# Performance work log

Measured on AMD Instinct MI355X. Metric: run time of the kernel, lower is better.

## Reference

```python
import jax, jax.numpy as jnp
import numpy as np

B, N, NI, H, QK, A = 1, 256, 64, 256, 128, 11
M = B * N

def _lstm_cell(x, h, c, w_ih, w_hh, b_ih, b_hh):
    # PyTorch LSTMCell gate order: i, f, g, o
    g = x @ w_ih.T + b_ih + h @ w_hh.T + b_hh
    i, f, gg, o = jnp.split(g, 4, axis=-1)
    c2 = jax.nn.sigmoid(f) * c + jax.nn.sigmoid(i) * jnp.tanh(gg)
    return jax.nn.sigmoid(o) * jnp.tanh(c2), c2

def _run_lstm(xs, w_ih, w_hh, b_ih, b_hh, reverse):
    # xs: (T, Bm, I); one direction of nn.LSTM with zero initial state
    Bm, Hh = xs.shape[1], w_hh.shape[1]
    def step(carry, x):
        h2, c2 = _lstm_cell(x, carry[0], carry[1], w_ih, w_hh, b_ih, b_hh)
        return (h2, c2), h2
    init = (jnp.zeros((Bm, Hh), xs.dtype), jnp.zeros((Bm, Hh), xs.dtype))
    return jax.lax.scan(step, init, xs, reverse=reverse)[1]

def setup_inputs():
    key = jax.random.key(0)
    ks = jax.random.split(key, 28)
    s = 0.1
    p = lambda k, sh: jax.random.normal(k, sh, jnp.float32) * s
    u = jax.random.uniform(ks[1], (M - 1, M, 2), jnp.float32, 1e-6, 1.0)
    return {
        "x": jax.random.normal(ks[0], (B, N, NI), jnp.float32),
        "h_in": jnp.zeros((M, H), jnp.float32),
        "c_in": jnp.zeros((M, H), jnp.float32),
        "gumbel": -jnp.log(-jnp.log(u)),
        "enc_w": p(ks[2], (H, NI)), "enc_b": p(ks[3], (H,)),
        "cell_w_ih": p(ks[4], (4 * H, H)), "cell_w_hh": p(ks[5], (4 * H, H)),
        "cell_b_ih": p(ks[6], (4 * H,)), "cell_b_hh": p(ks[7], (4 * H,)),
        "lf_w_ih": p(ks[8], (8 * H, 2 * H)), "lf_w_hh": p(ks[9], (8 * H, 2 * H)),
        "lf_b_ih": p(ks[10], (8 * H,)), "lf_b_hh": p(ks[11], (8 * H,)),
        "lr_w_ih": p(ks[12], (8 * H, 2 * H)), "lr_w_hh": p(ks[13], (8 * H, 2 * H)),
        "lr_b_ih": p(ks[14], (8 * H,)), "lr_b_hh": p(ks[15], (8 * H,)),
        "lin_w": p(ks[16], (2, 4 * H)), "lin_b": p(ks[17], (2,)),
        "wq_w": p(ks[18], (QK, H)), "wq_b": p(ks[19], (QK,)),
        "wk_w": p(ks[20], (QK, H)), "wk_b": p(ks[21], (QK,)),
        "val_w": p(ks[22], (1, 2 * H)), "val_b": p(ks[23], (1,)),
        "head_w": p(ks[24], (A, 2 * H)), "head_b": p(ks[25], (A,)),
    }

def _forward(x, h_in, c_in, gumbel, enc_w, enc_b, cell_w_ih, cell_w_hh, cell_b_ih, cell_b_hh,
             lf_w_ih, lf_w_hh, lf_b_ih, lf_b_hh, lr_w_ih, lr_w_hh, lr_b_ih, lr_b_hh,
             lin_w, lin_b, wq_w, wq_b, wk_w, wk_b, val_w, val_b, head_w, head_b):
    enc = x @ enc_w.T + enc_b                    # (B, N, H)
    inp = enc.reshape(M, H)
    h, c = _lstm_cell(inp, h_in, c_in, cell_w_ih, cell_w_hh, cell_b_ih, cell_b_hh)
    # idx[a, t] = t-th other agent for agent a (skips self) -- replaces the nested Python loops
    ar = jnp.arange(M - 1)[None, :]
    idx = ar + (ar >= jnp.arange(M)[:, None])    # (M, M-1) int
    pair = jnp.concatenate([jnp.broadcast_to(h[:, None, :], (M, M - 1, H)), h[idx]], axis=-1)
    hai = pair.transpose(1, 0, 2)                # (M-1, M, 2H), seq-major like torch stack(dim=1)
    y = jnp.concatenate([
        _run_lstm(hai, lf_w_ih, lf_w_hh, lf_b_ih, lf_b_hh, False),
        _run_lstm(hai, lr_w_ih, lr_w_hh, lr_b_ih, lr_b_hh, True)], axis=-1)  # (M-1, M, 4H)
    logits = y @ lin_w.T + lin_b                 # (M-1, M, 2)
    # hard gumbel-softmax (tau=1) with straight-through estimator
    ysoft = jax.nn.softmax(logits + gumbel, axis=-1)
    oh = jax.nn.one_hot(jnp.argmax(ysoft, axis=-1), 2, dtype=ysoft.dtype)
    gs = oh + ysoft - jax.lax.stop_gradient(ysoft)
    hard = gs[..., 1].transpose(1, 0)            # (M, M-1): narrow(dim=2,1,1) + permute + squeeze
    nz = jnp.count_nonzero(hard).astype(jnp.float32)
    d1 = nz / (N * N)
    d2 = nz / (N * (N - 1))
    q = h @ wq_w.T + wq_b
    k = h @ wk_w.T + wk_b
    sa = (q @ k.T) * (1.0 / float(np.sqrt(QK)))  # (M, M)
    sa = jnp.take_along_axis(sa, idx, axis=1) * hard   # drop diagonal, gate
    attn = jax.nn.softmax(sa, axis=1) * hard
    # agent_mask is all ones here (no 'alive_mask' in info), so masking is identity
    comm = jnp.einsum('mt,mth->mh', attn, h[idx])      # (M, H)
    val = jnp.concatenate([h, comm], axis=-1) @ val_w.T + val_b  # (M, 1)
    h3 = h.reshape(B, N, H)
    c3 = comm.reshape(B, N, H)
    act = jax.nn.log_softmax(jnp.concatenate([h3, c3], axis=-1) @ head_w.T + head_b, axis=-1)
    return act, val, h, c, jnp.stack([d1, d2])

def reference(x, h_in, c_in, gumbel, enc_w, enc_b, cell_w_ih, cell_w_hh, cell_b_ih, cell_b_hh,
              lf_w_ih, lf_w_hh, lf_b_ih, lf_b_hh, lr_w_ih, lr_w_hh, lr_b_ih, lr_b_hh,
              lin_w, lin_b, wq_w, wq_b, wk_w, wk_b, val_w, val_b, head_w, head_b):
    return _forward(x, h_in, c_in, gumbel, enc_w, enc_b, cell_w_ih, cell_w_hh, cell_b_ih, cell_b_hh,
                    lf_w_ih, lf_w_hh, lf_b_ih, lf_b_hh, lr_w_ih, lr_w_hh, lr_b_ih, lr_b_hh,
                    lin_w, lin_b, wq_w, wq_b, wk_w, wk_b, val_w, val_b, head_w, head_b)
```

## Files before the change

### kernel.cpp

```cpp
#include <hip/hip_runtime.h>
#include <hip/hip_bf16.h>

typedef float f32x4  __attribute__((ext_vector_type(4)));
typedef short s16x4  __attribute__((ext_vector_type(4)));
typedef short s16x8  __attribute__((ext_vector_type(8)));
typedef __bf16 bf16x8 __attribute__((ext_vector_type(8)));
typedef unsigned int u32;
typedef unsigned long long u64;

#define DEVI static __device__ __forceinline__

DEVI short f2bf(float f){
  u32 u = __builtin_bit_cast(u32,f);
  u += 0x7fffu + ((u>>16)&1u);
  return (short)(u>>16);
}
DEVI float sigm(float x){ return 1.f/(1.f+__expf(-x)); }
DEVI float tanh_(float x){ return 1.f - 2.f/(1.f+__expf(2.f*x)); }

DEVI bf16x8 ldbf8(const short* p){ return __builtin_bit_cast(bf16x8, *(const s16x8*)p); }

DEVI f32x4 cld16(const void* p){
  f32x4 r;
  asm volatile("global_load_dwordx4 %0, %1, off sc0 sc1" : "=v"(r) : "v"(p) : "memory");
  return r;
}
DEVI void cst8(void* p, u64 v){
  asm volatile("global_store_dwordx2 %0, %1, off sc0 sc1" :: "v"(p), "v"(v) : "memory");
}
DEVI void cst4(int* p, int v){
  asm volatile("global_store_dword %0, %1, off sc0 sc1" :: "v"(p), "v"(v) : "memory");
}
DEVI int cld4(const int* p){
  int r;
  asm volatile("global_load_dword %0, %1, off sc0 sc1\n\ts_waitcnt vmcnt(0)"
               : "=v"(r) : "v"(p) : "memory");
  return r;
}

#define NSTEP 255

#define WS_H1F      0u
#define WS_H1BF     262144u
#define WS_ABUF     393216u
#define WS_CELLW    655360u
#define WS_WIH      1703936u
#define WS_WPACK    5898240u
#define WS_GATES1   10092544u
#define WS_GX       11141120u
#define WS_HBUF     19529728u
#define WS_LDIFF    20578304u
#define WS_Q        28934144u
#define WS_K        29065216u
#define WS_SA       29196288u
#define WS_HARD     29458432u
#define WS_FLAGS    29719552u
#define WS_NZ       29723648u

__global__ void k_pack(const float* __restrict__ lf_whh, const float* __restrict__ lr_whh,
                       const float* __restrict__ cwih, const float* __restrict__ cwhh,
                       const float* __restrict__ lf_wih, const float* __restrict__ lr_wih,
                       short* __restrict__ wpack, short* __restrict__ cellw, short* __restrict__ wih)
{
  int bx = blockIdx.x, tid = threadIdx.x;
  if (bx < 1024) {
    int idx = bx*256 + tid;
    int lane = idx & 63;
    int kk   = (idx>>6)&15;
    int ct   = (idx>>10)&3;
    int w    = (idx>>12)&3;
    int hb8  = (idx>>14)&7;
    int d    = (idx>>17)&1;
    const float* W = d ? lr_whh : lf_whh;
    int wrow = 512*w + hb8*64 + ct*16 + (lane&15);
    short v[8];
    #pragma unroll
    for (int jj=0;jj<8;++jj){
      int k = 32*kk + 8*(lane>>4) + jj;
      v[jj] = f2bf(W[(size_t)wrow*512 + k]);
    }
    s16x8 o;
    #pragma unroll
    for (int jj=0;jj<8;++jj) o[jj] = v[jj];
    *(s16x8*)(wpack + (size_t)idx*8) = o;
  } else if (bx < 3072) {
    int e = (bx-1024)*256 + tid;
    int cg = e>>9, k = e&511;
    float val = (k<256) ? cwih[cg*256 + k] : cwhh[cg*256 + (k-256)];
    cellw[e] = f2bf(val);
  } else {
    int e = (bx-3072)*256 + tid;
    int d = e>>20, r = e & 1048575;
    const float* W = d ? lr_wih : lf_wih;
    wih[e] = f2bf(W[r]);
  }
}

__global__ void k1a(const float* __restrict__ x, const float* __restrict__ enc_w,
                    const float* __restrict__ enc_b, const float* __restrict__ h_in,
                    short* __restrict__ abuf)
{
  __shared__ float xs[64];
  int b = blockIdx.x, u = threadIdx.x;
  if (u < 64) xs[u] = x[b*64 + u];
  __syncthreads();
  float acc = enc_b[u];
  #pragma unroll 8
  for (int j=0;j<64;++j) acc += xs[j]*enc_w[u*64+j];
  abuf[b*512 + u]       = f2bf(acc);
  abuf[b*512 + 256 + u] = f2bf(h_in[b*256 + u]);
}

__global__ void k1b(const short* __restrict__ abuf, const short* __restrict__ cellw,
                    float* __restrict__ gates1)
{
  int tid = threadIdx.x, w = tid>>6, l = tid&63;
  int m0 = (blockIdx.x&3)*64 + 32*(w&1);
  int n0 = (blockIdx.x>>2)*64 + 32*(w>>1);
  int arow = l&15, ag = l>>4;
  f32x4 acc[2][2] = {};
  #pragma unroll 4
  for (int kk=0; kk<16; ++kk){
    int ko = 32*kk + 8*ag;
    bf16x8 a0 = ldbf8(abuf + (size_t)(m0 + arow)*512 + ko);
    bf16x8 a1 = ldbf8(abuf + (size_t)(m0 + 16 + arow)*512 + ko);
    bf16x8 b0 = ldbf8(cellw + (size_t)(n0 + arow)*512 + ko);
    bf16x8 b1 = ldbf8(cellw + (size_t)(n0 + 16 + arow)*512 + ko);
    acc[0][0] = __builtin_amdgcn_mfma_f32_16x16x32_bf16(a0,b0,acc[0][0],0,0,0);
    acc[0][1] = __builtin_amdgcn_mfma_f32_16x16x32_bf16(a0,b1,acc[0][1],0,0,0);
    acc[1][0] = __builtin_amdgcn_mfma_f32_16x16x32_bf16(a1,b0,acc[1][0],0,0,0);
    acc[1][1] = __builtin_amdgcn_mfma_f32_16x16x32_bf16(a1,b1,acc[1][1],0,0,0);
  }
  #pragma unroll
  for (int rt=0;rt<2;++rt)
    #pragma unroll
    for (int ct=0;ct<2;++ct)
      #pragma unroll
      for (int reg=0;reg<4;++reg)
        gates1[(size_t)(m0 + 16*rt + 4*ag + reg)*1024 + n0 + 16*ct + arow] = acc[rt][ct][reg];
}

__global__ void k1c(const float* __restrict__ gates1, const float* __restrict__ bih,
                    const float* __restrict__ bhh, const float* __restrict__ c_in,
                    float* __restrict__ out_h, float* __restrict__ out_c,
                    float* __restrict__ h1f, short* __restrict__ h1bf)
{
  int b = blockIdx.x, u = threadIdx.x;
  const float* g = gates1 + (size_t)b*1024;
  float iv = g[u]     + bih[u]     + bhh[u];
  float fv = g[256+u] + bih[256+u] + bhh[256+u];
  float gv = g[512+u] + bih[512+u] + bhh[512+u];
  float ov = g[768+u] + bih[768+u] + bhh[768+u];
  float c = sigm(fv)*c_in[b*256+u] + sigm(iv)*tanh_(gv);
  float h = sigm(ov)*tanh_(c);
  out_h[b*256+u] = h; out_c[b*256+u] = c;
  h1f[b*256+u] = h;   h1bf[b*256+u] = f2bf(h);
}

__global__ void k_qk(const float* __restrict__ h1, const float* __restrict__ wq_w,
                     const float* __restrict__ wq_b, const float* __restrict__ wk_w,
                     const float* __restrict__ wk_b, float* __restrict__ q, float* __restrict__ k)
{
  __shared__ float hrow[256];
  int b = blockIdx.x, u = threadIdx.x;
  hrow[u] = h1[b*256+u];
  hrow[u+128] = h1[b*256+u+128];
  __syncthreads();
  const float* W  = blockIdx.y ? wk_w : wq_w;
  const float* bb = blockIdx.y ? wk_b : wq_b;
  float* out = blockIdx.y ? k : q;
  float acc = bb[u];
  #pragma unroll 8
  for (int j=0;j<256;++j) acc += hrow[j]*W[u*256+j];
  out[b*128+u] = acc;
}

__global__ void k_sa(const float* __restrict__ q, const float* __restrict__ k, float* __restrict__ sa)
{
  __shared__ float qrow[128];
  int b = blockIdx.x, j = threadIdx.x;
  if (j < 128) qrow[j] = q[b*128+j];
  __syncthreads();
  float acc = 0.f;
  #pragma unroll 8
  for (int kk=0;kk<128;++kk) acc += qrow[kk]*k[j*128+kk];
  sa[b*256+j] = acc * 0.08838834764831845f;
}

__global__ void k_gx(const short* __restrict__ h1bf, const short* __restrict__ wih,
                     const float* __restrict__ lf_bih, const float* __restrict__ lf_bhh,
                     const float* __restrict__ lr_bih, const float* __restrict__ lr_bhh,
                     float* __restrict__ gx)
{
  int z = blockIdx.y, d = z>>1, half = z&1;
  int tid = threadIdx.x, w = tid>>6, l = tid&63;
  int m0 = (blockIdx.x&3)*64 + 32*(w&1);
  int n0 = (blockIdx.x>>2)*64 + 32*(w>>1);
  int arow = l&15, ag = l>>4;
  const short* Bb = wih + (size_t)d*2048*512 + 256*half;
  f32x4 acc[2][2] = {};
  #pragma unroll 4
  for (int kk=0;kk<8;++kk){
    int ko = 32*kk + 8*ag;
    bf16x8 a0 = ldbf8(h1bf + (size_t)(m0 + arow)*256 + ko);
    bf16x8 a1 = ldbf8(h1bf + (size_t)(m0 + 16 + arow)*256 + ko);
    bf16x8 b0 = ldbf8(Bb + (size_t)(n0 + arow)*512 + ko);
    bf16x8 b1 = ldbf8(Bb + (size_t)(n0 + 16 + arow)*512 + ko);
    acc[0][0] = __builtin_amdgcn_mfma_f32_16x16x32_bf16(a0,b0,acc[0][0],0,0,0);
    acc[0][1] = __builtin_amdgcn_mfma_f32_16x16x32_bf16(a0,b1,acc[0][1],0,0,0);
    acc[1][0] = __builtin_amdgcn_mfma_f32_16x16x32_bf16(a1,b0,acc[1][0],0,0,0);
    acc[1][1] = __builtin_amdgcn_mfma_f32_16x16x32_bf16(a1,b1,acc[1][1],0,0,0);
  }
  const float* bi = d ? lr_bih : lf_bih;
  const float* bh = d ? lr_bhh : lf_bhh;
  float* out = gx + (size_t)z*256*2048;
  #pragma unroll
  for (int rt=0;rt<2;++rt)
    #pragma unroll
    for (int ct=0;ct<2;++ct){
      int cg = n0 + 16*ct + arow;
      float bias = (half==0) ? (bi[cg] + bh[cg]) : 0.f;
      #pragma unroll
      for (int reg=0;reg<4;++reg)
        out[(size_t)(m0 + 16*rt + 4*ag + reg)*2048 + cg] = acc[rt][ct][reg] + bias;
    }
}

__global__ __launch_bounds__(256,1) void k_rec(
  const short* __restrict__ wpack, const float* __restrict__ gx,
  short* __restrict__ hbuf, float* __restrict__ ldiff,
  const float* __restrict__ lin_w, int* __restrict__ flags)
{
  __shared__ short h_lds[2][16*512];
  __shared__ float glds[2][4][16][68];
  const int tid = threadIdx.x;
  const int w = tid>>6, l = tid&63;
  const int bid = blockIdx.x;
  const int d   = bid>>7;
  const int g16 = (bid>>3)&15;
  const int hb8 = bid&7;
  const int r0  = g16*16;
  const int grp = d*16 + g16;

  bf16x8 breg[4][16];
  {
    const short* wp = wpack + (size_t)(((d*8+hb8)*4 + w)*4)*16*64*8 + (size_t)l*8;
    #pragma unroll
    for (int ct=0;ct<4;++ct)
      #pragma unroll
      for (int kk=0;kk<16;++kk)
        breg[ct][kk] = ldbf8(wp + (size_t)(ct*16+kk)*64*8);
  }

  const int r_e = tid>>4;
  const int j4  = (tid&15)*4;
  const int rg_e = r0 + r_e;
  float gx1c[16], ldwc[4];
  {
    const float* g1 = gx + ((size_t)(d*2)*256 + rg_e)*2048 + hb8*64 + j4;
    #pragma unroll
    for (int g=0;g<4;++g){
      f32x4 v = *(const f32x4*)(g1 + g*512);
      gx1c[g*4+0]=v.x; gx1c[g*4+1]=v.y; gx1c[g*4+2]=v.z; gx1c[g*4+3]=v.w;
    }
    #pragma unroll
    for (int jj=0;jj<4;++jj){
      int col = d*512 + hb8*64 + j4 + jj;
      ldwc[jj] = lin_w[1024+col] - lin_w[col];
    }
  }
  float c_st[4] = {0.f,0.f,0.f,0.f};
  int* slots  = flags + grp*32;
  int* myslot = slots + hb8*4 + w;
  const float* gx2base = gx + (size_t)(d*2+1)*256*2048 + hb8*64 + j4;

  const int s_row = tid>>4;
  const int c0    = tid&15;
  const int arow = l&15, ag = l>>4;

  for (int tau=0; tau<NSTEP; ++tau){
    const int t = d ? (254-tau) : tau;
    f32x4 x2r[4];
    {
      const float* g2 = gx2base + (size_t)(t + (t>=rg_e ? 1:0))*2048;
      #pragma unroll
      for (int g=0;g<4;++g) x2r[g] = *(const f32x4*)(g2 + g*512);
    }
    if (tau){
      int v = tau;
      do {
        if (l < 32) v = cld4(slots + l);
      } while (__any(v < tau));
    }
    const int p = tau&1;
    {
      const short* hsrc = hbuf + (size_t)((p*2+d)*256 + r0 + s_row)*512;
      f32x4 q[4];
      #pragma unroll
      for (int i=0;i<4;++i)
        q[i] = cld16(hsrc + (size_t)(c0 + 16*i)*8);
      asm volatile("s_waitcnt vmcnt(0)" ::: "memory");
      #pragma unroll
      for (int i=0;i<4;++i){
        int c = c0 + 16*i;
        int wb = (16*c) ^ ((s_row&15)<<4);
        *(f32x4*)((char*)h_lds[p] + s_row*1024 + wb) = q[i];
      }
    }
    __syncthreads();
    f32x4 acc[4] = {};
    #pragma unroll
    for (int kk=0;kk<16;++kk){
      int swz0 = (64*kk + 16*ag) ^ (arow<<4);
      bf16x8 a = __builtin_bit_cast(bf16x8, *(const s16x8*)((char*)h_lds[p] + arow*1024 + swz0));
      acc[0] = __builtin_amdgcn_mfma_f32_16x16x32_bf16(a,breg[0][kk],acc[0],0,0,0);
      acc[1] = __builtin_amdgcn_mfma_f32_16x16x32_bf16(a,breg[1][kk],acc[1],0,0,0);
      acc[2] = __builtin_amdgcn_mfma_f32_16x16x32_bf16(a,breg[2][kk],acc[2],0,0,0);
      acc[3] = __builtin_amdgcn_mfma_f32_16x16x32_bf16(a,breg[3][kk],acc[3],0,0,0);
    }
    #pragma unroll
    for (int ct=0;ct<4;++ct)
      #pragma unroll
      for (int reg=0;reg<4;++reg)
        glds[p][w][4*ag + reg][16*ct + arow] = acc[ct][reg];
    __syncthreads();
    {
      float gvals[16], hv[4];
      #pragma unroll
      for (int g=0; g<4; ++g){
        f32x4 mm = *(const f32x4*)&glds[p][g][r_e][j4];
        gvals[g*4+0] = mm.x + gx1c[g*4+0] + x2r[g].x;
        gvals[g*4+1] = mm.y + gx1c[g*4+1] + x2r[g].y;
        gvals[g*4+2] = mm.z + gx1c[g*4+2] + x2r[g].z;
        gvals[g*4+3] = mm.w + gx1c[g*4+3] + x2r[g].w;
      }
      #pragma unroll
      for (int jj=0;jj<4;++jj){
        float iv = sigm(gvals[jj]);
        float fv = sigm(gvals[4+jj]);
        float gg = tanh_(gvals[8+jj]);
        float ov = sigm(gvals[12+jj]);
        float cc = fv*c_st[jj] + iv*gg;
        c_st[jj] = cc;
        hv[jj] = ov*tanh_(cc);
      }
      short* hdst = hbuf + (size_t)(((p^1)*2+d)*256 + rg_e)*512 + hb8*64 + j4;
      u32 lo = (u32)(unsigned short)f2bf(hv[0]) | ((u32)(unsigned short)f2bf(hv[1])<<16);
      u32 hi = (u32)(unsigned short)f2bf(hv[2]) | ((u32)(unsigned short)f2bf(hv[3])<<16);
      cst8(hdst, (u64)lo | ((u64)hi << 32));
      asm volatile("s_waitcnt vmcnt(0)" ::: "memory");
      if (l==0)
        cst4(myslot, tau+1);
      float s = hv[0]*ldwc[0] + hv[1]*ldwc[1] + hv[2]*ldwc[2] + hv[3]*ldwc[3];
      s += __shfl_xor(s,1); s += __shfl_xor(s,2); s += __shfl_xor(s,4); s += __shfl_xor(s,8);
      if ((l&15)==0)
        ldiff[((size_t)t*16 + d*8 + hb8)*256 + rg_e] = s;
    }
  }
}

__global__ void k_hard(const float* __restrict__ ldiff, const float* __restrict__ lin_b,
                       const float* __restrict__ gumbel, float* __restrict__ hard,
                       int* __restrict__ nz)
{
  int t = blockIdx.x, b = threadIdx.x;
  float s = lin_b[1] - lin_b[0];
  #pragma unroll 8
  for (int k=0;k<16;++k) s += ldiff[((size_t)t*16 + k)*256 + b];
  const float* gp = gumbel + ((size_t)t*256 + b)*2;
  s += gp[1] - gp[0];
  int bit = (s > 0.f) ? 1 : 0;
  hard[(size_t)b*255 + t] = (float)bit;
  unsigned long long ball = __ballot(bit);
  __shared__ int cnt[4];
  if ((threadIdx.x & 63)==0) cnt[threadIdx.x>>6] = __popcll(ball);
  __syncthreads();
  if (threadIdx.x==0) atomicAdd(nz, cnt[0]+cnt[1]+cnt[2]+cnt[3]);
}

__global__ void k_attn(const float* __restrict__ h1, const float* __restrict__ sa,
                       const float* __restrict__ hard,
                       const float* __restrict__ val_w, const float* __restrict__ val_b,
                       const float* __restrict__ head_w, const float* __restrict__ head_b,
                       const int* __restrict__ nz,
                       float* __restrict__ out_act, float* __restrict__ out_val,
                       float* __restrict__ out_d)
{
  __shared__ float red[256];
  __shared__ float at[256];
  __shared__ float wred[4];
  __shared__ float logit[11];
  int b = blockIdx.x, u = threadIdx.x;
  float hd = 0.f, sc = -3.0e38f;
  if (u < 255){
    hd = hard[(size_t)b*255 + u];
    int jsel = u + (u>=b ? 1:0);
    sc = sa[b*256 + jsel] * hd;
  }
  red[u] = sc; __syncthreads();
  for (int st=128; st; st>>=1){ if (u<st) red[u] = fmaxf(red[u], red[u+st]); __syncthreads(); }
  float mx = red[0]; __syncthreads();
  float e = (u<255) ? __expf(sc - mx) : 0.f;
  red[u] = e; __syncthreads();
  for (int st=128; st; st>>=1){ if (u<st) red[u] += red[u+st]; __syncthreads(); }
  float inv = 1.f/red[0]; __syncthreads();
  at[u] = (u<255) ? e*inv*hd : 0.f;
  __syncthreads();
  float comm = 0.f;
  for (int t2=0; t2<255; ++t2){
    int jsel = t2 + (t2>=b ? 1:0);
    comm += at[t2] * h1[(size_t)jsel*256 + u];
  }
  float hb_ = h1[(size_t)b*256 + u];
  float pv = hb_*val_w[u] + comm*val_w[256+u];
  red[u] = pv; __syncthreads();
  for (int st=128; st; st>>=1){ if (u<st) red[u] += red[u+st]; __syncthreads(); }
  if (u==0) out_val[b] = red[0] + val_b[0];
  for (int a=0; a<11; ++a){
    float s = hb_*head_w[a*512+u] + comm*head_w[a*512+256+u];
    s += __shfl_xor(s,32); s += __shfl_xor(s,16); s += __shfl_xor(s,8);
    s += __shfl_xor(s,4);  s += __shfl_xor(s,2);  s += __shfl_xor(s,1);
    if ((u&63)==0) wred[u>>6] = s;
    __syncthreads();
    if (u==0) logit[a] = wred[0]+wred[1]+wred[2]+wred[3] + head_b[a];
    __syncthreads();
  }
  if (u==0){
    float m = logit[0];
    #pragma unroll
    for (int a=1;a<11;++a) m = fmaxf(m, logit[a]);
    float se = 0.f;
    #pragma unroll
    for (int a=0;a<11;++a) se += __expf(logit[a]-m);
    float ls = __logf(se);
    #pragma unroll
    for (int a=0;a<11;++a) out_act[(size_t)b*11 + a] = logit[a] - m - ls;
  }
  if (b==0 && u==0){
    float n = (float)(*nz);
    out_d[0] = n / 65536.f;
    out_d[1] = n / 65280.f;
  }
}

extern "C" void kernel_launch(void* const* d_in, const int* in_sizes, int n_in,
                              void* d_out, int out_size, void* d_ws, size_t ws_size,
                              hipStream_t stream)
{
  const float* x      = (const float*)d_in[0];
  const float* h_in   = (const float*)d_in[1];
  const float* c_in   = (const float*)d_in[2];
  const float* gumbel = (const float*)d_in[3];
  const float* enc_w  = (const float*)d_in[4];
  const float* enc_b  = (const float*)d_in[5];
  const float* cwih   = (const float*)d_in[6];
  const float* cwhh   = (const float*)d_in[7];
  const float* cbih   = (const float*)d_in[8];
  const float* cbhh   = (const float*)d_in[9];
  const float* lf_wih = (const float*)d_in[10];
  const float* lf_whh = (const float*)d_in[11];
  const float* lf_bih = (const float*)d_in[12];
  const float* lf_bhh = (const float*)d_in[13];
  const float* lr_wih = (const float*)d_in[14];
  const float* lr_whh = (const float*)d_in[15];
  const float* lr_bih = (const float*)d_in[16];
  const float* lr_bhh = (const float*)d_in[17];
  const float* lin_w  = (const float*)d_in[18];
  const float* lin_b  = (const float*)d_in[19];
  const float* wq_w   = (const float*)d_in[20];
  const float* wq_b   = (const float*)d_in[21];
  const float* wk_w   = (const float*)d_in[22];
  const float* wk_b   = (const float*)d_in[23];
  const float* val_w  = (const float*)d_in[24];
  const float* val_b  = (const float*)d_in[25];
  const float* head_w = (const float*)d_in[26];
  const float* head_b = (const float*)d_in[27];

  char* ws = (char*)d_ws;
  float* h1f   = (float*)(ws + WS_H1F);
  short* h1bf  = (short*)(ws + WS_H1BF);
  short* abuf  = (short*)(ws + WS_ABUF);
  short* cellw = (short*)(ws + WS_CELLW);
  short* wih   = (short*)(ws + WS_WIH);
  short* wpack = (short*)(ws + WS_WPACK);
  float* gates1= (float*)(ws + WS_GATES1);
  float* gx    = (float*)(ws + WS_GX);
  short* hbuf  = (short*)(ws + WS_HBUF);
  float* ldiff = (float*)(ws + WS_LDIFF);
  float* qb    = (float*)(ws + WS_Q);
  float* kb    = (float*)(ws + WS_K);
  float* sab   = (float*)(ws + WS_SA);
  float* hardb = (float*)(ws + WS_HARD);
  int*   flags = (int*)(ws + WS_FLAGS);
  int*   nz    = (int*)(ws + WS_NZ);

  float* out_act = (float*)d_out;
  float* out_val = out_act + 2816;
  float* out_h   = out_val + 256;
  float* out_c   = out_h + 65536;
  float* out_d   = out_c + 65536;

  hipMemsetAsync(flags, 0, 4100, stream);
  hipMemsetAsync(hbuf, 0, 1048576, stream);

  k_pack<<<11264, 256, 0, stream>>>(lf_whh, lr_whh, cwih, cwhh, lf_wih, lr_wih, wpack, cellw, wih);
  k1a <<<256, 256, 0, stream>>>(x, enc_w, enc_b, h_in, abuf);
  k1b <<<64, 256, 0, stream>>>(abuf, cellw, gates1);
  k1c <<<256, 256, 0, stream>>>(gates1, cbih, cbhh, c_in, out_h, out_c, h1f, h1bf);
  k_qk<<<dim3(256,2), 128, 0, stream>>>(h1f, wq_w, wq_b, wk_w, wk_b, qb, kb);
  k_sa<<<256, 256, 0, stream>>>(qb, kb, sab);
  k_gx<<<dim3(128,4), 256, 0, stream>>>(h1bf, wih, lf_bih, lf_bhh, lr_bih, lr_bhh, gx);
  k_rec<<<256, 256, 0, stream>>>(wpack, gx, hbuf, ldiff, lin_w, flags);
  k_hard<<<255, 256, 0, stream>>>(ldiff, lin_b, gumbel, hardb, nz);
  k_attn<<<256, 256, 0, stream>>>(h1f, sab, hardb, val_w, val_b, head_w, head_b, nz,
                                  out_act, out_val, out_d);
}
```

Before: 1.050 ms.

## Replace flag polling with checksum-tagged hidden-state validation in recurrent kernel

Drops the separate step counter flags in the recurrence and their ordering. Producers no longer wait for the hidden-state store to complete before raising a flag. Instead, each wave publishes an XOR checksum of its hidden-state block, salted with a per-step golden-ratio value. Consumers load the hidden-state data and tags together and spin until the recomputed checksums match. This removes one full store-wait-then-poll round trip per timestep. In exchange, correctness becomes probabilistic: a checksum collision could accept stale data, and a bounded spin limit silently proceeds with whatever was loaded.

```diff
diff --git a/kernel.cpp b/kernel.cpp
--- a/kernel.cpp
+++ b/kernel.cpp
@@ -25,19 +25,16 @@
   asm volatile("global_load_dwordx4 %0, %1, off sc0 sc1" : "=v"(r) : "v"(p) : "memory");
   return r;
 }
+DEVI u64 cld8(const void* p){
+  u64 r;
+  asm volatile("global_load_dwordx2 %0, %1, off sc0 sc1" : "=v"(r) : "v"(p) : "memory");
+  return r;
+}
 DEVI void cst8(void* p, u64 v){
   asm volatile("global_store_dwordx2 %0, %1, off sc0 sc1" :: "v"(p), "v"(v) : "memory");
 }
-DEVI void cst4(int* p, int v){
-  asm volatile("global_store_dword %0, %1, off sc0 sc1" :: "v"(p), "v"(v) : "memory");
-}
-DEVI int cld4(const int* p){
-  int r;
-  asm volatile("global_load_dword %0, %1, off sc0 sc1\n\ts_waitcnt vmcnt(0)"
-               : "=v"(r) : "v"(p) : "memory");
-  return r;
-}
-
+
+#define GOLD 0x9E3779B97F4A7C15ull
 #define NSTEP 255
 
 #define WS_H1F      0u
@@ -54,8 +51,8 @@
 #define WS_K        29065216u
 #define WS_SA       29196288u
 #define WS_HARD     29458432u
-#define WS_FLAGS    29719552u
-#define WS_NZ       29723648u
+#define WS_TAGS     29719552u
+#define WS_NZ       29727744u
 
 __global__ void k_pack(const float* __restrict__ lf_whh, const float* __restrict__ lr_whh,
                        const float* __restrict__ cwih, const float* __restrict__ cwhh,
@@ -229,7 +226,7 @@
 __global__ __launch_bounds__(256,1) void k_rec(
   const short* __restrict__ wpack, const float* __restrict__ gx,
   short* __restrict__ hbuf, float* __restrict__ ldiff,
-  const float* __restrict__ lin_w, int* __restrict__ flags)
+  const float* __restrict__ lin_w, u64* __restrict__ tags)
 {
   __shared__ short h_lds[2][16*512];
   __shared__ float glds[2][4][16][68];
@@ -270,13 +267,13 @@
     }
   }
   float c_st[4] = {0.f,0.f,0.f,0.f};
-  int* slots  = flags + grp*32;
-  int* myslot = slots + hb8*4 + w;
+  u64* tgrp  = tags + (size_t)grp*32 + (size_t)w*8;
   const float* gx2base = gx + (size_t)(d*2+1)*256*2048 + hb8*64 + j4;
 
   const int s_row = tid>>4;
   const int c0    = tid&15;
   const int arow = l&15, ag = l>>4;
+  u64 vh = 0;
 
   for (int tau=0; tau<NSTEP; ++tau){
     const int t = d ? (254-tau) : tau;
@@ -286,26 +283,38 @@
       #pragma unroll
       for (int g=0;g<4;++g) x2r[g] = *(const f32x4*)(g2 + g*512);
     }
-    if (tau){
-      int v = tau;
-      do {
-        if (l < 32) v = cld4(slots + l);
-      } while (__any(v < tau));
-    }
     const int p = tau&1;
+    f32x4 q[4];
     {
       const short* hsrc = hbuf + (size_t)((p*2+d)*256 + r0 + s_row)*512;
-      f32x4 q[4];
-      #pragma unroll
-      for (int i=0;i<4;++i)
-        q[i] = cld16(hsrc + (size_t)(c0 + 16*i)*8);
-      asm volatile("s_waitcnt vmcnt(0)" ::: "memory");
-      #pragma unroll
-      for (int i=0;i<4;++i){
-        int c = c0 + 16*i;
-        int wb = (16*c) ^ ((s_row&15)<<4);
-        *(f32x4*)((char*)h_lds[p] + s_row*1024 + wb) = q[i];
+      u64 tg = 0;
+      int spins = 0;
+      for (;;){
+        #pragma unroll
+        for (int i=0;i<4;++i)
+          q[i] = cld16(hsrc + (size_t)(c0 + 16*i)*8);
+        if (l < 8) tg = cld8(tgrp + l);
+        asm volatile("s_waitcnt vmcnt(0)" ::: "memory");
+        bool ok = true;
+        #pragma unroll
+        for (int k=0;k<4;++k){
+          ulonglong2 u2 = __builtin_bit_cast(ulonglong2, q[k]);
+          u64 cz = u2.x ^ u2.y;
+          cz ^= __shfl_xor(cz,1); cz ^= __shfl_xor(cz,2); cz ^= __shfl_xor(cz,4);
+          cz ^= __shfl_xor(cz,16); cz ^= __shfl_xor(cz,32);
+          int blk = 2*k + ((l>>3)&1);
+          u64 tb = __shfl(tg, blk);
+          ok = ok && ((cz ^ vh) == tb);
+        }
+        if (__all(ok)) break;
+        if (++spins > (1<<22)) break;
       }
+    }
+    #pragma unroll
+    for (int i=0;i<4;++i){
+      int c = c0 + 16*i;
+      int wb = (16*c) ^ ((s_row&15)<<4);
+      *(f32x4*)((char*)h_lds[p] + s_row*1024 + wb) = q[i];
     }
     __syncthreads();
     f32x4 acc[4] = {};
@@ -347,15 +356,19 @@
       short* hdst = hbuf + (size_t)(((p^1)*2+d)*256 + rg_e)*512 + hb8*64 + j4;
       u32 lo = (u32)(unsigned short)f2bf(hv[0]) | ((u32)(unsigned short)f2bf(hv[1])<<16);
       u32 hi = (u32)(unsigned short)f2bf(hv[2]) | ((u32)(unsigned short)f2bf(hv[3])<<16);
-      cst8(hdst, (u64)lo | ((u64)hi << 32));
-      asm volatile("s_waitcnt vmcnt(0)" ::: "memory");
+      u64 pk = (u64)lo | ((u64)hi << 32);
+      cst8(hdst, pk);
+      u64 cks = pk;
+      cks ^= __shfl_xor(cks,1); cks ^= __shfl_xor(cks,2); cks ^= __shfl_xor(cks,4);
+      cks ^= __shfl_xor(cks,8); cks ^= __shfl_xor(cks,16); cks ^= __shfl_xor(cks,32);
       if (l==0)
-        cst4(myslot, tau+1);
+        cst8(tags + (size_t)grp*32 + (size_t)w*8 + hb8, cks ^ (vh + GOLD));
       float s = hv[0]*ldwc[0] + hv[1]*ldwc[1] + hv[2]*ldwc[2] + hv[3]*ldwc[3];
       s += __shfl_xor(s,1); s += __shfl_xor(s,2); s += __shfl_xor(s,4); s += __shfl_xor(s,8);
       if ((l&15)==0)
         ldiff[((size_t)t*16 + d*8 + hb8)*256 + rg_e] = s;
     }
+    vh += GOLD;
   }
 }
 
@@ -491,7 +504,7 @@
   float* kb    = (float*)(ws + WS_K);
   float* sab   = (float*)(ws + WS_SA);
   float* hardb = (float*)(ws + WS_HARD);
-  int*   flags = (int*)(ws + WS_FLAGS);
+  u64*   tags  = (u64*)(ws + WS_TAGS);
   int*   nz    = (int*)(ws + WS_NZ);
 
   float* out_act = (float*)d_out;
@@ -500,7 +513,7 @@
   float* out_c   = out_h + 65536;
   float* out_d   = out_c + 65536;
 
-  hipMemsetAsync(flags, 0, 4100, stream);
+  hipMemsetAsync(tags, 0, 8192 + 4, stream);
   hipMemsetAsync(hbuf, 0, 1048576, stream);
 
   k_pack<<<11264, 256, 0, stream>>>(lf_whh, lr_whh, cwih, cwhh, lf_wih, lr_wih, wpack, cellw, wih);
@@ -510,7 +523,7 @@
   k_qk<<<dim3(256,2), 128, 0, stream>>>(h1f, wq_w, wq_b, wk_w, wk_b, qb, kb);
   k_sa<<<256, 256, 0, stream>>>(qb, kb, sab);
   k_gx<<<dim3(128,4), 256, 0, stream>>>(h1bf, wih, lf_bih, lf_bhh, lr_bih, lr_bhh, gx);
-  k_rec<<<256, 256, 0, stream>>>(wpack, gx, hbuf, ldiff, lin_w, flags);
+  k_rec<<<256, 256, 0, stream>>>(wpack, gx, hbuf, ldiff, lin_w, tags);
   k_hard<<<255, 256, 0, stream>>>(ldiff, lin_b, gumbel, hardb, nz);
   k_attn<<<256, 256, 0, stream>>>(h1f, sab, hardb, val_w, val_b, head_w, head_b, nz,
                                   out_act, out_val, out_d);
```

Result: slower. 1.295 ms (+23.4%).

## Replace flag-based inter-block sync with versioned data+shadow validation in recurrence

Applied to the files above, without the earlier changes.

The persistent LSTM recurrence kernel no longer publishes per-wave step flags and spins on them before reading the shared hidden state. Each block now writes its bf16 h values together with a shadow copy XORed with a per-step version key, and readers poll the data and shadow until they match the expected version. This removes the store-wait-flag round trip and the separate flag polling, and it also drops the flag and hbuf memsets by zeroing LDS at step 0. The shadow buffer reuses the gates1 workspace. There is a small chance of a false match, and a bounded spin exits without a proper error if the check never passes.

```diff
diff --git a/kernel.cpp b/kernel.cpp
--- a/kernel.cpp
+++ b/kernel.cpp
@@ -28,16 +28,8 @@
 DEVI void cst8(void* p, u64 v){
   asm volatile("global_store_dwordx2 %0, %1, off sc0 sc1" :: "v"(p), "v"(v) : "memory");
 }
-DEVI void cst4(int* p, int v){
-  asm volatile("global_store_dword %0, %1, off sc0 sc1" :: "v"(p), "v"(v) : "memory");
-}
-DEVI int cld4(const int* p){
-  int r;
-  asm volatile("global_load_dword %0, %1, off sc0 sc1\n\ts_waitcnt vmcnt(0)"
-               : "=v"(r) : "v"(p) : "memory");
-  return r;
-}
-
+
+#define GOLD 0x9E3779B97F4A7C15ull
 #define NSTEP 255
 
 #define WS_H1F      0u
@@ -54,7 +46,6 @@
 #define WS_K        29065216u
 #define WS_SA       29196288u
 #define WS_HARD     29458432u
-#define WS_FLAGS    29719552u
 #define WS_NZ       29723648u
 
 __global__ void k_pack(const float* __restrict__ lf_whh, const float* __restrict__ lr_whh,
@@ -228,8 +219,8 @@
 
 __global__ __launch_bounds__(256,1) void k_rec(
   const short* __restrict__ wpack, const float* __restrict__ gx,
-  short* __restrict__ hbuf, float* __restrict__ ldiff,
-  const float* __restrict__ lin_w, int* __restrict__ flags)
+  short* __restrict__ hbuf, char* __restrict__ shadow,
+  float* __restrict__ ldiff, const float* __restrict__ lin_w)
 {
   __shared__ short h_lds[2][16*512];
   __shared__ float glds[2][4][16][68];
@@ -240,7 +231,6 @@
   const int g16 = (bid>>3)&15;
   const int hb8 = bid&7;
   const int r0  = g16*16;
-  const int grp = d*16 + g16;
 
   bf16x8 breg[4][16];
   {
@@ -270,36 +260,53 @@
     }
   }
   float c_st[4] = {0.f,0.f,0.f,0.f};
-  int* slots  = flags + grp*32;
-  int* myslot = slots + hb8*4 + w;
   const float* gx2base = gx + (size_t)(d*2+1)*256*2048 + hb8*64 + j4;
 
   const int s_row = tid>>4;
   const int c0    = tid&15;
   const int arow = l&15, ag = l>>4;
+  u64 vst = 0;
 
   for (int tau=0; tau<NSTEP; ++tau){
     const int t = d ? (254-tau) : tau;
+    const u64 vread = vst;
+    vst += GOLD;
     f32x4 x2r[4];
     {
       const float* g2 = gx2base + (size_t)(t + (t>=rg_e ? 1:0))*2048;
       #pragma unroll
       for (int g=0;g<4;++g) x2r[g] = *(const f32x4*)(g2 + g*512);
     }
-    if (tau){
-      int v = tau;
-      do {
-        if (l < 32) v = cld4(slots + l);
-      } while (__any(v < tau));
-    }
     const int p = tau&1;
-    {
-      const short* hsrc = hbuf + (size_t)((p*2+d)*256 + r0 + s_row)*512;
-      f32x4 q[4];
-      #pragma unroll
-      for (int i=0;i<4;++i)
-        q[i] = cld16(hsrc + (size_t)(c0 + 16*i)*8);
-      asm volatile("s_waitcnt vmcnt(0)" ::: "memory");
+    if (tau == 0){
+      f32x4 z = {};
+      #pragma unroll
+      for (int i=0;i<4;++i){
+        int c = c0 + 16*i;
+        int wb = (16*c) ^ ((s_row&15)<<4);
+        *(f32x4*)((char*)h_lds[p] + s_row*1024 + wb) = z;
+      }
+    } else {
+      const char* dsrc = (const char*)(hbuf + (size_t)((p*2+d)*256 + r0 + s_row)*512);
+      const char* ssrc = shadow + ((size_t)((p*2+d)*256 + r0 + s_row)*512)*2;
+      f32x4 q[4], sh[4];
+      u32 vm = 0;
+      for (int it=0;;++it){
+        #pragma unroll
+        for (int i=0;i<4;++i) if (!((vm>>i)&1u)){
+          q[i]  = cld16(dsrc + (size_t)(c0+16*i)*16);
+          sh[i] = cld16(ssrc + (size_t)(c0+16*i)*16);
+        }
+        asm volatile("s_waitcnt vmcnt(0)" ::: "memory");
+        #pragma unroll
+        for (int i=0;i<4;++i) if (!((vm>>i)&1u)){
+          ulonglong2 dq = __builtin_bit_cast(ulonglong2, q[i]);
+          ulonglong2 sq = __builtin_bit_cast(ulonglong2, sh[i]);
+          if (((dq.x ^ sq.x) == vread) && ((dq.y ^ sq.y) == vread)) vm |= (1u<<i);
+        }
+        if (__all(vm == 15u)) break;
+        if (it > (1<<20)) break;
+      }
       #pragma unroll
       for (int i=0;i<4;++i){
         int c = c0 + 16*i;
@@ -344,13 +351,14 @@
         c_st[jj] = cc;
         hv[jj] = ov*tanh_(cc);
       }
-      short* hdst = hbuf + (size_t)(((p^1)*2+d)*256 + rg_e)*512 + hb8*64 + j4;
-      u32 lo = (u32)(unsigned short)f2bf(hv[0]) | ((u32)(unsigned short)f2bf(hv[1])<<16);
-      u32 hi = (u32)(unsigned short)f2bf(hv[2]) | ((u32)(unsigned short)f2bf(hv[3])<<16);
-      cst8(hdst, (u64)lo | ((u64)hi << 32));
-      asm volatile("s_waitcnt vmcnt(0)" ::: "memory");
-      if (l==0)
-        cst4(myslot, tau+1);
+      if (tau < NSTEP-1){
+        size_t boff = ((size_t)(((p^1)*2+d)*256 + rg_e)*512 + hb8*64 + j4) * 2;
+        u32 lo = (u32)(unsigned short)f2bf(hv[0]) | ((u32)(unsigned short)f2bf(hv[1])<<16);
+        u32 hi = (u32)(unsigned short)f2bf(hv[2]) | ((u32)(unsigned short)f2bf(hv[3])<<16);
+        u64 pk = (u64)lo | ((u64)hi << 32);
+        cst8((char*)hbuf + boff, pk);
+        cst8(shadow + boff, pk ^ vst);
+      }
       float s = hv[0]*ldwc[0] + hv[1]*ldwc[1] + hv[2]*ldwc[2] + hv[3]*ldwc[3];
       s += __shfl_xor(s,1); s += __shfl_xor(s,2); s += __shfl_xor(s,4); s += __shfl_xor(s,8);
       if ((l&15)==0)
@@ -491,7 +499,6 @@
   float* kb    = (float*)(ws + WS_K);
   float* sab   = (float*)(ws + WS_SA);
   float* hardb = (float*)(ws + WS_HARD);
-  int*   flags = (int*)(ws + WS_FLAGS);
   int*   nz    = (int*)(ws + WS_NZ);
 
   float* out_act = (float*)d_out;
@@ -500,8 +507,7 @@
   float* out_c   = out_h + 65536;
   float* out_d   = out_c + 65536;
 
-  hipMemsetAsync(flags, 0, 4100, stream);
-  hipMemsetAsync(hbuf, 0, 1048576, stream);
+  hipMemsetAsync(nz, 0, 4, stream);
 
   k_pack<<<11264, 256, 0, stream>>>(lf_whh, lr_whh, cwih, cwhh, lf_wih, lr_wih, wpack, cellw, wih);
   k1a <<<256, 256, 0, stream>>>(x, enc_w, enc_b, h_in, abuf);
@@ -510,7 +516,7 @@
   k_qk<<<dim3(256,2), 128, 0, stream>>>(h1f, wq_w, wq_b, wk_w, wk_b, qb, kb);
   k_sa<<<256, 256, 0, stream>>>(qb, kb, sab);
   k_gx<<<dim3(128,4), 256, 0, stream>>>(h1bf, wih, lf_bih, lf_bhh, lr_bih, lr_bhh, gx);
-  k_rec<<<256, 256, 0, stream>>>(wpack, gx, hbuf, ldiff, lin_w, flags);
+  k_rec<<<256, 256, 0, stream>>>(wpack, gx, hbuf, (char*)gates1, ldiff, lin_w);
   k_hard<<<255, 256, 0, stream>>>(ldiff, lin_b, gumbel, hardb, nz);
   k_attn<<<256, 256, 0, stream>>>(h1f, sab, hardb, val_w, val_b, head_w, head_b, nz,
                                   out_act, out_val, out_d);
```

After: 957.6 us (median of 2 runs). 8.8% less time.
